# Optimization experiments

Hardware: AMD Instinct MI355X
Metric: run time of the kernel (lower is better)

## Reference

```python
import jax, jax.numpy as jnp
import numpy as np

LATENT = 16
HID = 512
N_CLASSES = 10
STYLE = 64
B = 8192


def _he(key, shape, fan_in):
    return jax.random.normal(key, shape, dtype=jnp.float32) * jnp.sqrt(2.0 / fan_in)


def setup_inputs() -> dict:
    key = jax.random.key(0)
    ks = jax.random.split(key, 20)
    inp = {}
    inp['z'] = jax.random.normal(ks[0], (B, LATENT), dtype=jnp.float32)
    inp['y'] = jax.random.randint(ks[1], (B,), 0, N_CLASSES)
    inp['sw0'] = _he(ks[2], (LATENT, HID), LATENT)
    inp['sb0'] = jnp.zeros((HID,), jnp.float32)
    inp['sw1'] = _he(ks[3], (HID, HID), HID)
    inp['sb1'] = jnp.zeros((HID,), jnp.float32)
    inp['sw2'] = _he(ks[4], (HID, HID), HID)
    inp['sb2'] = jnp.zeros((HID,), jnp.float32)
    inp['sw3'] = _he(ks[5], (HID, HID), HID)
    inp['sb3'] = jnp.zeros((HID,), jnp.float32)
    # unshared per-class experts stacked on leading class axis C
    inp['uw0'] = _he(ks[6], (N_CLASSES, HID, HID), HID)
    inp['ub0'] = jnp.zeros((N_CLASSES, HID), jnp.float32)
    inp['uw1'] = _he(ks[7], (N_CLASSES, HID, HID), HID)
    inp['ub1'] = jnp.zeros((N_CLASSES, HID), jnp.float32)
    inp['uw2'] = _he(ks[8], (N_CLASSES, HID, HID), HID)
    inp['ub2'] = jnp.zeros((N_CLASSES, HID), jnp.float32)
    inp['uw3'] = _he(ks[9], (N_CLASSES, HID, STYLE), HID)
    inp['ub3'] = jnp.zeros((N_CLASSES, STYLE), jnp.float32)
    return inp


def reference(z, y, sw0, sb0, sw1, sb1, sw2, sb2, sw3, sb3,
              uw0, ub0, uw1, ub1, uw2, ub2, uw3, ub3):
    # shared trunk: 4 Linear+ReLU
    h = jax.nn.relu(z @ sw0 + sb0)
    h = jax.nn.relu(h @ sw1 + sb1)
    h = jax.nn.relu(h @ sw2 + sb2)
    h = jax.nn.relu(h @ sw3 + sb3)          # [B, H]
    # all per-class expert branches (matches original dense computation)
    o = jax.nn.relu(jnp.einsum('bd,cde->bce', h, uw0) + ub0)   # [B, C, H]
    o = jax.nn.relu(jnp.einsum('bcd,cde->bce', o, uw1) + ub1)
    o = jax.nn.relu(jnp.einsum('bcd,cde->bce', o, uw2) + ub2)
    out = jnp.einsum('bcd,cds->bcs', o, uw3) + ub3             # [B, C, S], no ReLU
    # gather the branch matching each sample's class
    s = out[jnp.arange(out.shape[0]), y]                        # [B, S]
    return s
```

## Files before the change

### kernel.cpp

```cpp
#include <hip/hip_runtime.h>

#define B_SAMPLES 8192
#define HID       512
#define NCLS      10
#define STYLE_D   64
#define LATENT_D  16

#define BM 128
#define BN 64
#define BK 64
#define MAXT    (B_SAMPLES/BM + NCLS)
#define MAXROWS (B_SAMPLES + NCLS*BM)

typedef short v8s __attribute__((ext_vector_type(8)));
typedef float v4f __attribute__((ext_vector_type(4)));

__device__ __forceinline__ short f2bf(float f) {
    union { float f; unsigned u; } x; x.f = f;
    unsigned r = x.u + 0x7fffu + ((x.u >> 16) & 1u);
    return (short)(r >> 16);
}

__device__ __forceinline__ void gload16(const short* g, short* l) {
    __builtin_amdgcn_global_load_lds(
        (const __attribute__((address_space(1))) void*)g,
        (__attribute__((address_space(3))) void*)l, 16, 0, 0);
}

__device__ __forceinline__ int kswz(int row, int k) {
    return (k & ~63) + ((((k >> 3) & 7) ^ (row & 7)) << 3) + (k & 7);
}
__device__ __forceinline__ int cswz(int key, int n0, int c) {
    return n0 + ((((c >> 3) ^ key) & 7) << 3) + (c & 7);
}

__global__ void build_groups(const int* __restrict__ y, int* __restrict__ tclass,
                             int* __restrict__ trow0, int* __restrict__ order,
                             int* __restrict__ rank) {
    __shared__ int cnt[NCLS], cur[NCLS];
    int t = threadIdx.x;
    if (t < NCLS) cnt[t] = 0;
    __syncthreads();
    for (int b = t; b < B_SAMPLES; b += 1024) atomicAdd(&cnt[y[b]], 1);
    __syncthreads();
    if (t == 0) {
        int off = 0, tt = 0;
        for (int c = 0; c < NCLS; ++c) {
            cur[c] = off;
            int nt = (cnt[c] + BM - 1) / BM;
            for (int j = 0; j < nt; ++j) { tclass[tt] = c; trow0[tt] = off + j * BM; ++tt; }
            off += nt * BM;
        }
        for (int u = tt; u < MAXT; ++u) { tclass[u] = -1; trow0[u] = 0; }
    }
    __syncthreads();
    for (int i = t; i < MAXROWS; i += 1024) order[i] = -1;
    __syncthreads();
    for (int b = t; b < B_SAMPLES; b += 1024) {
        int c = y[b];
        int p = atomicAdd(&cur[c], 1);
        order[p] = b;
        rank[b] = p;
    }
}

__global__ void prep_zb(const float* __restrict__ z, short* __restrict__ zb) {
    int idx = blockIdx.x * 256 + threadIdx.x;
    int b = idx >> 6, k = idx & 63;
    zb[b * 64 + kswz(b, k)] = f2bf(k < LATENT_D ? z[(size_t)b * LATENT_D + k] : 0.f);
}

__global__ void transpose_mega(const float* __restrict__ sw0, const float* __restrict__ sw1,
                               const float* __restrict__ sw2, const float* __restrict__ sw3,
                               const float* __restrict__ uw0, const float* __restrict__ uw1,
                               const float* __restrict__ uw2, const float* __restrict__ uw3,
                               short* __restrict__ wt0, short* __restrict__ wt1,
                               short* __restrict__ wt2, short* __restrict__ wt3,
                               short* __restrict__ wtu0, short* __restrict__ wtu1,
                               short* __restrict__ wtu2, short* __restrict__ wtu3) {
    __shared__ float tile[32][33];
    int zz = blockIdx.z;
    int tx = threadIdx.x, ty = threadIdx.y;
    if (zz == 34) {
        if (blockIdx.x >= 16 || blockIdx.y >= 2) return;
        int n0 = blockIdx.x * 32, k0 = blockIdx.y * 32;
        #pragma unroll
        for (int j = 0; j < 32; j += 8) {
            int k = k0 + ty + j;
            tile[ty + j][tx] = (k < LATENT_D) ? sw0[(size_t)k * HID + n0 + tx] : 0.f;
        }
        __syncthreads();
        #pragma unroll
        for (int j = 0; j < 32; j += 8) {
            int n = n0 + ty + j, k = k0 + tx;
            wt0[n * 64 + kswz(n, k)] = f2bf(tile[tx][ty + j]);
        }
        return;
    }
    if (zz == 33) {
        int cls = blockIdx.x >> 1;
        int n0 = (blockIdx.x & 1) * 32, k0 = blockIdx.y * 32;
        const float* s = uw3  + (size_t)cls * HID * STYLE_D;
        short*       d = wtu3 + (size_t)cls * STYLE_D * HID;
        #pragma unroll
        for (int j = 0; j < 32; j += 8)
            tile[ty + j][tx] = s[(size_t)(k0 + ty + j) * STYLE_D + n0 + tx];
        __syncthreads();
        #pragma unroll
        for (int j = 0; j < 32; j += 8) {
            int n = n0 + ty + j, k = k0 + tx;
            d[(size_t)n * HID + kswz(n, k)] = f2bf(tile[tx][ty + j]);
        }
        return;
    }
    if (blockIdx.x >= 16) return;
    const float* s; short* d;
    if      (zz == 0) { s = sw1; d = wt1; }
    else if (zz == 1) { s = sw2; d = wt2; }
    else if (zz == 2) { s = sw3; d = wt3; }
    else if (zz < 13) { size_t o = (size_t)(zz - 3)  * HID * HID; s = uw0 + o; d = wtu0 + o; }
    else if (zz < 23) { size_t o = (size_t)(zz - 13) * HID * HID; s = uw1 + o; d = wtu1 + o; }
    else              { size_t o = (size_t)(zz - 23) * HID * HID; s = uw2 + o; d = wtu2 + o; }
    int n0 = blockIdx.x * 32, k0 = blockIdx.y * 32;
    #pragma unroll
    for (int j = 0; j < 32; j += 8)
        tile[ty + j][tx] = s[(size_t)(k0 + ty + j) * HID + n0 + tx];
    __syncthreads();
    #pragma unroll
    for (int j = 0; j < 32; j += 8) {
        int n = n0 + ty + j, k = k0 + tx;
        d[(size_t)n * HID + kswz(n, k)] = f2bf(tile[tx][ty + j]);
    }
}

template <int MODE>
__global__ __launch_bounds__(256, 2) void gemm2ph(
    const short* __restrict__ A, const short* __restrict__ WT,
    const float* __restrict__ bias, void* __restrict__ Outv,
    const int N, const int K, const long wStride, const int biasN,
    const int* __restrict__ aux, const int* __restrict__ tclass,
    const int* __restrict__ trow0) {

    const unsigned gx = gridDim.x;
    const unsigned nwg = gx * gridDim.y;
    {
        unsigned lin = blockIdx.x + gx * blockIdx.y;
        unsigned q = nwg >> 3, r = nwg & 7, xcd = lin & 7, idx = lin >> 3;
        unsigned wgid = (xcd < r ? xcd * (q + 1) : r * (q + 1) + (xcd - r) * q) + idx;
        lin = wgid;
        unsigned bx = lin % gx, by = lin / gx;
        int tile = by, cls = 0, row0;
        if (MODE <= 1) {
            row0 = tile * BM;
        } else {
            cls = tclass[tile];
            if (cls < 0) return;
            row0 = trow0[tile];
        }
        const int n0 = bx * BN;
        const short* wt = WT + (size_t)cls * wStride;
        const float* bs = bias + (size_t)cls * biasN;

        __shared__ short As[2][BM * BK];
        __shared__ short Bs[2][BN * BK];

        const int t = threadIdx.x, lane = t & 63, w = t >> 6;
        const int srow = lane >> 3, scol = (lane & 7) * 8;
        const int wr = w >> 1, wc = w & 1;
        const int lrow = lane & 15, lko = lane >> 4;
        const int key = lrow & 7;

        v4f acc[4][2] = {};

        auto stage = [&](int buf, int k0) {
            #pragma unroll
            for (int p = 0; p < 4; ++p) {
                int row = p * 32 + w * 8 + srow;
                gload16(A + (size_t)(row0 + row) * K + k0 + scol, &As[buf][p * 2048 + w * 512]);
            }
            #pragma unroll
            for (int q2 = 0; q2 < 2; ++q2) {
                int row = q2 * 32 + w * 8 + srow;
                gload16(wt + (size_t)(n0 + row) * K + k0 + scol, &Bs[buf][q2 * 2048 + w * 512]);
            }
        };

        stage(0, 0);
        __syncthreads();
        const int nk = K / BK;
        for (int ks = 0; ks < nk; ++ks) {
            int buf = ks & 1;
            if (ks + 1 < nk) stage(buf ^ 1, (ks + 1) * BK);

            #pragma unroll
            for (int kk = 0; kk < 2; ++kk) {
                int ch = ((kk * 4 + lko) ^ key) << 3;
                v8s af[4], bq[2];
                #pragma unroll
                for (int i = 0; i < 4; ++i)
                    af[i] = *(const v8s*)&As[buf][(wr * 64 + i * 16 + lrow) * BK + ch];
                #pragma unroll
                for (int j = 0; j < 2; ++j)
                    bq[j] = *(const v8s*)&Bs[buf][(wc * 32 + j * 16 + lrow) * BK + ch];
                #pragma unroll
                for (int i = 0; i < 4; ++i)
                    #pragma unroll
                    for (int j = 0; j < 2; ++j)
                        acc[i][j] = __builtin_amdgcn_mfma_f32_16x16x32_bf16(
                            af[i], bq[j], acc[i][j], 0, 0, 0);
            }
            __syncthreads();
        }

        #pragma unroll
        for (int i = 0; i < 4; ++i)
            #pragma unroll
            for (int j = 0; j < 2; ++j)
                #pragma unroll
                for (int q3 = 0; q3 < 4; ++q3) {
                    int rr = wr * 64 + i * 16 + lko * 4 + q3;
                    int c = wc * 32 + j * 16 + lrow;
                    if (MODE == 3) {
                        int o = aux[row0 + rr];
                        if (o >= 0)
                            ((float*)Outv)[(size_t)o * STYLE_D + n0 + c] = acc[i][j][q3] + bs[n0 + c];
                    } else {
                        float v = fmaxf(acc[i][j][q3] + bs[n0 + c], 0.f);
                        int orow = (MODE == 1) ? aux[row0 + rr] : (row0 + rr);
                        ((short*)Outv)[(size_t)orow * N + cswz(orow & 7, n0, c)] = f2bf(v);
                    }
                }
    }
}

extern "C" void kernel_launch(void* const* d_in, const int* in_sizes, int n_in,
                              void* d_out, int out_size, void* d_ws, size_t ws_size,
                              hipStream_t stream) {
    const float* z   = (const float*)d_in[0];
    const int*   y   = (const int*)d_in[1];
    const float* sw0 = (const float*)d_in[2];
    const float* sb0 = (const float*)d_in[3];
    const float* sw1 = (const float*)d_in[4];
    const float* sb1 = (const float*)d_in[5];
    const float* sw2 = (const float*)d_in[6];
    const float* sb2 = (const float*)d_in[7];
    const float* sw3 = (const float*)d_in[8];
    const float* sb3 = (const float*)d_in[9];
    const float* uw0 = (const float*)d_in[10];
    const float* ub0 = (const float*)d_in[11];
    const float* uw1 = (const float*)d_in[12];
    const float* ub1 = (const float*)d_in[13];
    const float* uw2 = (const float*)d_in[14];
    const float* ub2 = (const float*)d_in[15];
    const float* uw3 = (const float*)d_in[16];
    const float* ub3 = (const float*)d_in[17];

    char* p = (char*)d_ws;
    auto alloc = [&](size_t bytes) -> char* {
        char* r = p; p += (bytes + 255) & ~(size_t)255; return r;
    };
    int*   tclass = (int*)alloc(MAXT * 4);
    int*   trow0  = (int*)alloc(MAXT * 4);
    int*   order  = (int*)alloc(MAXROWS * 4);
    int*   rank   = (int*)alloc(B_SAMPLES * 4);
    short* zb     = (short*)alloc((size_t)B_SAMPLES * 64 * 2);
    short* wt0    = (short*)alloc((size_t)HID * 64 * 2);
    short* wt1    = (short*)alloc((size_t)HID * HID * 2);
    short* wt2    = (short*)alloc((size_t)HID * HID * 2);
    short* wt3    = (short*)alloc((size_t)HID * HID * 2);
    short* wtu0   = (short*)alloc((size_t)NCLS * HID * HID * 2);
    short* wtu1   = (short*)alloc((size_t)NCLS * HID * HID * 2);
    short* wtu2   = (short*)alloc((size_t)NCLS * HID * HID * 2);
    short* wtu3   = (short*)alloc((size_t)NCLS * STYLE_D * HID * 2);
    short* act0   = (short*)alloc((size_t)MAXROWS * HID * 2);
    short* act1   = (short*)alloc((size_t)MAXROWS * HID * 2);
    short* act2   = (short*)alloc((size_t)MAXROWS * HID * 2);

    build_groups<<<1, 1024, 0, stream>>>(y, tclass, trow0, order, rank);
    prep_zb<<<(B_SAMPLES * 64) / 256, 256, 0, stream>>>(z, zb);
    dim3 tb(32, 8);
    transpose_mega<<<dim3(20, 16, 35), tb, 0, stream>>>(
        sw0, sw1, sw2, sw3, uw0, uw1, uw2, uw3,
        wt0, wt1, wt2, wt3, wtu0, wtu1, wtu2, wtu3);

    gemm2ph<0><<<dim3(HID / BN, B_SAMPLES / BM), 256, 0, stream>>>(
        zb, wt0, sb0, act0, HID, 64, 0, 0, nullptr, nullptr, nullptr);
    gemm2ph<0><<<dim3(HID / BN, B_SAMPLES / BM), 256, 0, stream>>>(
        act0, wt1, sb1, act1, HID, HID, 0, 0, nullptr, nullptr, nullptr);
    gemm2ph<0><<<dim3(HID / BN, B_SAMPLES / BM), 256, 0, stream>>>(
        act1, wt2, sb2, act0, HID, HID, 0, 0, nullptr, nullptr, nullptr);
    gemm2ph<1><<<dim3(HID / BN, B_SAMPLES / BM), 256, 0, stream>>>(
        act0, wt3, sb3, act2, HID, HID, 0, 0, rank, nullptr, nullptr);

    gemm2ph<2><<<dim3(HID / BN, MAXT), 256, 0, stream>>>(
        act2, wtu0, ub0, act0, HID, HID, (long)HID * HID, HID,
        nullptr, tclass, trow0);
    gemm2ph<2><<<dim3(HID / BN, MAXT), 256, 0, stream>>>(
        act0, wtu1, ub1, act1, HID, HID, (long)HID * HID, HID,
        nullptr, tclass, trow0);
    gemm2ph<2><<<dim3(HID / BN, MAXT), 256, 0, stream>>>(
        act1, wtu2, ub2, act0, HID, HID, (long)HID * HID, HID,
        nullptr, tclass, trow0);
    gemm2ph<3><<<dim3(1, MAXT), 256, 0, stream>>>(
        act0, wtu3, ub3, d_out, HID, HID, (long)STYLE_D * HID, STYLE_D,
        order, tclass, trow0);
}
```

Before: 114.7 us.

## Triple-buffer GEMM K-loop with explicit vmcnt waits and fold z prep into transpose

Replaces the double-buffered GEMM with a three-stage LDS ring that prefetches two K-tiles ahead. It uses hand-placed s_waitcnt vmcnt and raw s_barrier instead of __syncthreads, raises wave priority around the MFMA section, and makes K a template constant so the loop fully unrolls. Separately, the z-to-bf16 prep kernel is merged into the transpose launch as an extra z-slice, saving one launch. The change increases LDS use, which may lower occupancy, and depends on the vmcnt counts matching the number of issued loads.

```diff
diff --git a/kernel.cpp b/kernel.cpp
--- a/kernel.cpp
+++ b/kernel.cpp
@@ -64,16 +64,12 @@
     }
 }
 
-__global__ void prep_zb(const float* __restrict__ z, short* __restrict__ zb) {
-    int idx = blockIdx.x * 256 + threadIdx.x;
-    int b = idx >> 6, k = idx & 63;
-    zb[b * 64 + kswz(b, k)] = f2bf(k < LATENT_D ? z[(size_t)b * LATENT_D + k] : 0.f);
-}
-
-__global__ void transpose_mega(const float* __restrict__ sw0, const float* __restrict__ sw1,
+__global__ void transpose_mega(const float* __restrict__ z,
+                               const float* __restrict__ sw0, const float* __restrict__ sw1,
                                const float* __restrict__ sw2, const float* __restrict__ sw3,
                                const float* __restrict__ uw0, const float* __restrict__ uw1,
                                const float* __restrict__ uw2, const float* __restrict__ uw3,
+                               short* __restrict__ zb,
                                short* __restrict__ wt0, short* __restrict__ wt1,
                                short* __restrict__ wt2, short* __restrict__ wt3,
                                short* __restrict__ wtu0, short* __restrict__ wtu1,
@@ -81,6 +77,16 @@
     __shared__ float tile[32][33];
     int zz = blockIdx.z;
     int tx = threadIdx.x, ty = threadIdx.y;
+    if (zz == 35) {
+        int t = ty * 32 + tx;
+        int base = (blockIdx.y * 20 + blockIdx.x) * 256 + t;
+        for (int i = base; i < B_SAMPLES * 64; i += 320 * 256) {
+            int b = i >> 6, k = i & 63;
+            zb[b * 64 + kswz(b, k)] =
+                f2bf(k < LATENT_D ? z[(size_t)b * LATENT_D + k] : 0.f);
+        }
+        return;
+    }
     if (zz == 34) {
         if (blockIdx.x >= 16 || blockIdx.y >= 2) return;
         int n0 = blockIdx.x * 32, k0 = blockIdx.y * 32;
@@ -133,104 +139,119 @@
     }
 }
 
-template <int MODE>
-__global__ __launch_bounds__(256, 2) void gemm2ph(
+template <int MODE, int NK>
+__global__ __launch_bounds__(256, 2) void gemm3s(
     const short* __restrict__ A, const short* __restrict__ WT,
     const float* __restrict__ bias, void* __restrict__ Outv,
-    const int N, const int K, const long wStride, const int biasN,
+    const int N, const long wStride, const int biasN,
     const int* __restrict__ aux, const int* __restrict__ tclass,
     const int* __restrict__ trow0) {
 
+    constexpr int K = NK * BK;
     const unsigned gx = gridDim.x;
     const unsigned nwg = gx * gridDim.y;
+    unsigned lin = blockIdx.x + gx * blockIdx.y;
     {
-        unsigned lin = blockIdx.x + gx * blockIdx.y;
         unsigned q = nwg >> 3, r = nwg & 7, xcd = lin & 7, idx = lin >> 3;
-        unsigned wgid = (xcd < r ? xcd * (q + 1) : r * (q + 1) + (xcd - r) * q) + idx;
-        lin = wgid;
-        unsigned bx = lin % gx, by = lin / gx;
-        int tile = by, cls = 0, row0;
-        if (MODE <= 1) {
-            row0 = tile * BM;
-        } else {
-            cls = tclass[tile];
-            if (cls < 0) return;
-            row0 = trow0[tile];
-        }
-        const int n0 = bx * BN;
-        const short* wt = WT + (size_t)cls * wStride;
-        const float* bs = bias + (size_t)cls * biasN;
-
-        __shared__ short As[2][BM * BK];
-        __shared__ short Bs[2][BN * BK];
-
-        const int t = threadIdx.x, lane = t & 63, w = t >> 6;
-        const int srow = lane >> 3, scol = (lane & 7) * 8;
-        const int wr = w >> 1, wc = w & 1;
-        const int lrow = lane & 15, lko = lane >> 4;
-        const int key = lrow & 7;
-
-        v4f acc[4][2] = {};
-
-        auto stage = [&](int buf, int k0) {
+        lin = (xcd < r ? xcd * (q + 1) : r * (q + 1) + (xcd - r) * q) + idx;
+    }
+    const unsigned bx = lin % gx, by = lin / gx;
+
+    int tile = by, cls = 0, row0;
+    if (MODE <= 1) {
+        row0 = tile * BM;
+    } else {
+        cls = tclass[tile];
+        if (cls < 0) return;
+        row0 = trow0[tile];
+    }
+    const int n0 = bx * BN;
+    const short* wt = WT + (size_t)cls * wStride;
+    const float* bs = bias + (size_t)cls * biasN;
+
+    __shared__ short As[3][BM * BK];
+    __shared__ short Bs[3][BN * BK];
+
+    const int t = threadIdx.x, lane = t & 63, w = t >> 6;
+    const int srow = lane >> 3, scol = (lane & 7) * 8;
+    const int wr = w >> 1, wc = w & 1;
+    const int lrow = lane & 15, lko = lane >> 4;
+    const int key = lrow & 7;
+
+    v4f acc[4][2] = {};
+
+    auto stage = [&](int buf, int k0) {
+        #pragma unroll
+        for (int p = 0; p < 4; ++p) {
+            int row = p * 32 + w * 8 + srow;
+            gload16(A + (size_t)(row0 + row) * K + k0 + scol, &As[buf][p * 2048 + w * 512]);
+        }
+        #pragma unroll
+        for (int q2 = 0; q2 < 2; ++q2) {
+            int row = q2 * 32 + w * 8 + srow;
+            gload16(wt + (size_t)(n0 + row) * K + k0 + scol, &Bs[buf][q2 * 2048 + w * 512]);
+        }
+    };
+
+    stage(0, 0);
+    if (NK > 1) stage(1, BK);
+
+    #pragma unroll
+    for (int ks = 0; ks < NK; ++ks) {
+        const int buf = ks % 3;
+        if (ks + 2 < NK) stage((ks + 2) % 3, (ks + 2) * BK);
+
+        if (ks <= NK - 3)      asm volatile("s_waitcnt vmcnt(12)" ::: "memory");
+        else if (ks == NK - 2) asm volatile("s_waitcnt vmcnt(6)"  ::: "memory");
+        else                   asm volatile("s_waitcnt vmcnt(0)"  ::: "memory");
+        __builtin_amdgcn_sched_barrier(0);
+        __builtin_amdgcn_s_barrier();
+        __builtin_amdgcn_sched_barrier(0);
+
+        __builtin_amdgcn_s_setprio(1);
+        #pragma unroll
+        for (int kk = 0; kk < 2; ++kk) {
+            int ch = ((kk * 4 + lko) ^ key) << 3;
+            v8s af[4], bq[2];
             #pragma unroll
-            for (int p = 0; p < 4; ++p) {
-                int row = p * 32 + w * 8 + srow;
-                gload16(A + (size_t)(row0 + row) * K + k0 + scol, &As[buf][p * 2048 + w * 512]);
-            }
+            for (int i = 0; i < 4; ++i)
+                af[i] = *(const v8s*)&As[buf][(wr * 64 + i * 16 + lrow) * BK + ch];
             #pragma unroll
-            for (int q2 = 0; q2 < 2; ++q2) {
-                int row = q2 * 32 + w * 8 + srow;
-                gload16(wt + (size_t)(n0 + row) * K + k0 + scol, &Bs[buf][q2 * 2048 + w * 512]);
-            }
-        };
-
-        stage(0, 0);
-        __syncthreads();
-        const int nk = K / BK;
-        for (int ks = 0; ks < nk; ++ks) {
-            int buf = ks & 1;
-            if (ks + 1 < nk) stage(buf ^ 1, (ks + 1) * BK);
-
+            for (int j = 0; j < 2; ++j)
+                bq[j] = *(const v8s*)&Bs[buf][(wc * 32 + j * 16 + lrow) * BK + ch];
             #pragma unroll
-            for (int kk = 0; kk < 2; ++kk) {
-                int ch = ((kk * 4 + lko) ^ key) << 3;
-                v8s af[4], bq[2];
-                #pragma unroll
-                for (int i = 0; i < 4; ++i)
-                    af[i] = *(const v8s*)&As[buf][(wr * 64 + i * 16 + lrow) * BK + ch];
+            for (int i = 0; i < 4; ++i)
                 #pragma unroll
                 for (int j = 0; j < 2; ++j)
-                    bq[j] = *(const v8s*)&Bs[buf][(wc * 32 + j * 16 + lrow) * BK + ch];
-                #pragma unroll
-                for (int i = 0; i < 4; ++i)
-                    #pragma unroll
-                    for (int j = 0; j < 2; ++j)
-                        acc[i][j] = __builtin_amdgcn_mfma_f32_16x16x32_bf16(
-                            af[i], bq[j], acc[i][j], 0, 0, 0);
+                    acc[i][j] = __builtin_amdgcn_mfma_f32_16x16x32_bf16(
+                        af[i], bq[j], acc[i][j], 0, 0, 0);
+        }
+        __builtin_amdgcn_s_setprio(0);
+
+        asm volatile("s_waitcnt lgkmcnt(0)" ::: "memory");
+        __builtin_amdgcn_sched_barrier(0);
+        __builtin_amdgcn_s_barrier();
+        __builtin_amdgcn_sched_barrier(0);
+    }
+
+    #pragma unroll
+    for (int i = 0; i < 4; ++i)
+        #pragma unroll
+        for (int j = 0; j < 2; ++j)
+            #pragma unroll
+            for (int q3 = 0; q3 < 4; ++q3) {
+                int rr = wr * 64 + i * 16 + lko * 4 + q3;
+                int c = wc * 32 + j * 16 + lrow;
+                if (MODE == 3) {
+                    int o = aux[row0 + rr];
+                    if (o >= 0)
+                        ((float*)Outv)[(size_t)o * STYLE_D + n0 + c] = acc[i][j][q3] + bs[n0 + c];
+                } else {
+                    float v = fmaxf(acc[i][j][q3] + bs[n0 + c], 0.f);
+                    int orow = (MODE == 1) ? aux[row0 + rr] : (row0 + rr);
+                    ((short*)Outv)[(size_t)orow * N + cswz(orow & 7, n0, c)] = f2bf(v);
+                }
             }
-            __syncthreads();
-        }
-
-        #pragma unroll
-        for (int i = 0; i < 4; ++i)
-            #pragma unroll
-            for (int j = 0; j < 2; ++j)
-                #pragma unroll
-                for (int q3 = 0; q3 < 4; ++q3) {
-                    int rr = wr * 64 + i * 16 + lko * 4 + q3;
-                    int c = wc * 32 + j * 16 + lrow;
-                    if (MODE == 3) {
-                        int o = aux[row0 + rr];
-                        if (o >= 0)
-                            ((float*)Outv)[(size_t)o * STYLE_D + n0 + c] = acc[i][j][q3] + bs[n0 + c];
-                    } else {
-                        float v = fmaxf(acc[i][j][q3] + bs[n0 + c], 0.f);
-                        int orow = (MODE == 1) ? aux[row0 + rr] : (row0 + rr);
-                        ((short*)Outv)[(size_t)orow * N + cswz(orow & 7, n0, c)] = f2bf(v);
-                    }
-                }
-    }
 }
 
 extern "C" void kernel_launch(void* const* d_in, const int* in_sizes, int n_in,
@@ -277,31 +298,26 @@
     short* act2   = (short*)alloc((size_t)MAXROWS * HID * 2);
 
     build_groups<<<1, 1024, 0, stream>>>(y, tclass, trow0, order, rank);
-    prep_zb<<<(B_SAMPLES * 64) / 256, 256, 0, stream>>>(z, zb);
     dim3 tb(32, 8);
-    transpose_mega<<<dim3(20, 16, 35), tb, 0, stream>>>(
-        sw0, sw1, sw2, sw3, uw0, uw1, uw2, uw3,
-        wt0, wt1, wt2, wt3, wtu0, wtu1, wtu2, wtu3);
-
-    gemm2ph<0><<<dim3(HID / BN, B_SAMPLES / BM), 256, 0, stream>>>(
-        zb, wt0, sb0, act0, HID, 64, 0, 0, nullptr, nullptr, nullptr);
-    gemm2ph<0><<<dim3(HID / BN, B_SAMPLES / BM), 256, 0, stream>>>(
-        act0, wt1, sb1, act1, HID, HID, 0, 0, nullptr, nullptr, nullptr);
-    gemm2ph<0><<<dim3(HID / BN, B_SAMPLES / BM), 256, 0, stream>>>(
-        act1, wt2, sb2, act0, HID, HID, 0, 0, nullptr, nullptr, nullptr);
-    gemm2ph<1><<<dim3(HID / BN, B_SAMPLES / BM), 256, 0, stream>>>(
-        act0, wt3, sb3, act2, HID, HID, 0, 0, rank, nullptr, nullptr);
-
-    gemm2ph<2><<<dim3(HID / BN, MAXT), 256, 0, stream>>>(
-        act2, wtu0, ub0, act0, HID, HID, (long)HID * HID, HID,
-        nullptr, tclass, trow0);
-    gemm2ph<2><<<dim3(HID / BN, MAXT), 256, 0, stream>>>(
-        act0, wtu1, ub1, act1, HID, HID, (long)HID * HID, HID,
-        nullptr, tclass, trow0);
-    gemm2ph<2><<<dim3(HID / BN, MAXT), 256, 0, stream>>>(
-        act1, wtu2, ub2, act0, HID, HID, (long)HID * HID, HID,
-        nullptr, tclass, trow0);
-    gemm2ph<3><<<dim3(1, MAXT), 256, 0, stream>>>(
-        act0, wtu3, ub3, d_out, HID, HID, (long)STYLE_D * HID, STYLE_D,
-        order, tclass, trow0);
-}
+    transpose_mega<<<dim3(20, 16, 36), tb, 0, stream>>>(
+        z, sw0, sw1, sw2, sw3, uw0, uw1, uw2, uw3,
+        zb, wt0, wt1, wt2, wt3, wtu0, wtu1, wtu2, wtu3);
+
+    gemm3s<0, 1><<<dim3(HID / BN, B_SAMPLES / BM), 256, 0, stream>>>(
+        zb, wt0, sb0, act0, HID, 0, 0, nullptr, nullptr, nullptr);
+    gemm3s<0, 8><<<dim3(HID / BN, B_SAMPLES / BM), 256, 0, stream>>>(
+        act0, wt1, sb1, act1, HID, 0, 0, nullptr, nullptr, nullptr);
+    gemm3s<0, 8><<<dim3(HID / BN, B_SAMPLES / BM), 256, 0, stream>>>(
+        act1, wt2, sb2, act0, HID, 0, 0, nullptr, nullptr, nullptr);
+    gemm3s<1, 8><<<dim3(HID / BN, B_SAMPLES / BM), 256, 0, stream>>>(
+        act0, wt3, sb3, act2, HID, 0, 0, rank, nullptr, nullptr);
+
+    gemm3s<2, 8><<<dim3(HID / BN, MAXT), 256, 0, stream>>>(
+        act2, wtu0, ub0, act0, HID, (long)HID * HID, HID, nullptr, tclass, trow0);
+    gemm3s<2, 8><<<dim3(HID / BN, MAXT), 256, 0, stream>>>(
+        act0, wtu1, ub1, act1, HID, (long)HID * HID, HID, nullptr, tclass, trow0);
+    gemm3s<2, 8><<<dim3(HID / BN, MAXT), 256, 0, stream>>>(
+        act1, wtu2, ub2, act0, HID, (long)HID * HID, HID, nullptr, tclass, trow0);
+    gemm3s<3, 8><<<dim3(1, MAXT), 256, 0, stream>>>(
+        act0, wtu3, ub3, d_out, HID, (long)STYLE_D * HID, STYLE_D, order, tclass, trow0);
+}
```

New measurement: 123.1 us. +7.3%, slower.
